# Performance work log

Hardware: AMD Instinct MI355X
Metric: run time of the kernel (lower is better)

## Reference

```python
import jax, jax.numpy as jnp
import numpy as np

B, LQ, LK = 8, 64, 256
E, H, D, NH = 128, 4, 32, 128  # embed_time, num_heads, input_dim, nhidden
EK = E // H


def setup_inputs() -> dict:
    key = jax.random.key(0)
    ks = jax.random.split(key, 10)
    s = 1.0 / np.sqrt(E)
    so = 1.0 / np.sqrt(D * H)
    return {
        "query": jax.random.normal(ks[0], (B, LQ, E), jnp.float32),
        "key": jax.random.normal(ks[1], (B, LK, E), jnp.float32),
        "value": jax.random.normal(ks[2], (B, LK, D), jnp.float32),
        "mask": jax.random.randint(ks[3], (B, LK, D), 0, 2, jnp.int32),
        "Wq": jax.random.uniform(ks[4], (E, E), jnp.float32, -s, s),
        "bq": jax.random.uniform(ks[5], (E,), jnp.float32, -s, s),
        "Wk": jax.random.uniform(ks[6], (E, E), jnp.float32, -s, s),
        "bk": jax.random.uniform(ks[7], (E,), jnp.float32, -s, s),
        "Wo": jax.random.uniform(ks[8], (D * H, NH), jnp.float32, -so, so),
        "bo": jax.random.uniform(ks[9], (NH,), jnp.float32, -so, so),
    }


def reference(query, key, value, mask, Wq, bq, Wk, bk, Wo, bo):
    # project and split heads: [B, L, E] -> [B, H, L, EK]
    q = (query @ Wq + bq).reshape(B, LQ, H, EK).transpose(0, 2, 1, 3)
    k = (key @ Wk + bk).reshape(B, LK, H, EK).transpose(0, 2, 1, 3)
    # scores: [B, H, LQ, LK]
    scores = jnp.einsum("bhqe,bhke->bhqk", q, k) / jnp.sqrt(jnp.asarray(EK, q.dtype))
    # per-feature masked logits: [B, H, LQ, LK, D] (broadcast, matches repeat_interleave)
    m = mask[:, None, None, :, :]  # [B,1,1,LK,D]
    logits = jnp.where(m == 0, jnp.asarray(-1e9, q.dtype), scores[..., None])
    p = jax.nn.softmax(logits, axis=-2)  # softmax over LK, per feature channel
    # weighted sum over LK: [B, H, LQ, D]
    x = jnp.sum(p * value[:, None, None, :, :], axis=-2)
    # merge heads: [B, LQ, H*D]
    x = x.transpose(0, 2, 1, 3).reshape(B, LQ, H * D)
    return x @ Wo + bo
```

## Files before the change

kernel.cpp:

```cpp
#include <hip/hip_runtime.h>

#define B_ 8
#define LQ_ 64
#define LK_ 256
#define E_ 128
#define H_ 4
#define D_ 32
#define NH_ 128
#define EK_ 32

__global__ __launch_bounds__(512) void fused_attn_kernel(
    const float* __restrict__ query, const float* __restrict__ key,
    const float* __restrict__ value, const int* __restrict__ mask,
    const float* __restrict__ Wq, const float* __restrict__ bq,
    const float* __restrict__ Wk,
    const float* __restrict__ Wo, const float* __restrict__ bo,
    float* __restrict__ out)
{
    const int blk = blockIdx.x;
    const int b  = blk >> 5;
    const int q0 = (blk & 31) * 2;
    const int t  = threadIdx.x;

    __shared__ float e_lds[8 * LK_];
    __shared__ float smem[9472];

    float* qrow  = smem;
    float* qpart = smem + 256;
    float* qp    = smem + 768;
    float* g     = smem + 1024;
    float* spart = smem + 2048;
    float* nump  = smem;
    float* denp  = smem + 4096;
    float* x     = smem + 8192;
    float* opart = smem + 8448;

    const int d  = t & 31;
    const int kg = t >> 5;
    float vv[16], mfv[16];
    {
        const float* vb = value + ((size_t)(b * LK_) + kg * 16) * D_ + d;
        const int*   mb = mask  + ((size_t)(b * LK_) + kg * 16) * D_ + d;
        #pragma unroll
        for (int j = 0; j < 16; ++j) {
            vv[j]  = vb[j * D_];
            mfv[j] = (float)mb[j * D_];
        }
    }

    if (t < 64) {
        reinterpret_cast<float4*>(qrow)[t] =
            reinterpret_cast<const float4*>(query + ((size_t)(b * LQ_) + q0) * E_)[t];
    }
    __syncthreads();

    {
        const int col = t & 127;
        const int z   = t >> 7;
        const int r   = z & 1;
        const int eh  = z >> 1;
        const float4* qr4 = reinterpret_cast<const float4*>(qrow + r * 128 + eh * 64);
        const float* wq = Wq + (size_t)(eh * 64) * E_ + col;
        float acc = 0.0f;
        #pragma unroll
        for (int j = 0; j < 16; ++j) {
            float4 qv = qr4[j];
            acc = fmaf(qv.x, wq[(size_t)(j * 4 + 0) * E_], acc);
            acc = fmaf(qv.y, wq[(size_t)(j * 4 + 1) * E_], acc);
            acc = fmaf(qv.z, wq[(size_t)(j * 4 + 2) * E_], acc);
            acc = fmaf(qv.w, wq[(size_t)(j * 4 + 3) * E_], acc);
        }
        qpart[z * 128 + col] = acc;
    }
    __syncthreads();

    if (t < 256) {
        const int col = t & 127, r = t >> 7;
        qp[r * 128 + col] =
            qpart[r * 128 + col] + qpart[(2 + r) * 128 + col] + bq[col];
    }
    __syncthreads();

    {
        const float inv_sqrt_ek = 0.17677669529663687f;
        const int e = t >> 2;
        const int p = t & 3;
        const float4* wk4 = reinterpret_cast<const float4*>(Wk + (size_t)e * E_ + p * EK_);
        float4 w[8];
        #pragma unroll
        for (int j = 0; j < 8; ++j) w[j] = wk4[j];
        #pragma unroll
        for (int r = 0; r < 2; ++r) {
            const float4* qp4 = reinterpret_cast<const float4*>(qp + r * 128 + p * EK_);
            float acc = 0.0f;
            #pragma unroll
            for (int j = 0; j < 8; ++j) {
                float4 pv = qp4[j];
                acc = fmaf(w[j].x, pv.x, acc);
                acc = fmaf(w[j].y, pv.y, acc);
                acc = fmaf(w[j].z, pv.z, acc);
                acc = fmaf(w[j].w, pv.w, acc);
            }
            g[(r * 4 + p) * 128 + e] = acc * inv_sqrt_ek;
        }
    }
    __syncthreads();

    {
        const int k  = t & 255;
        const int eh = t >> 8;
        const float4* kr =
            reinterpret_cast<const float4*>(key + ((size_t)(b * LK_) + k) * E_ + eh * 64);
        float acc[8] = {0.f, 0.f, 0.f, 0.f, 0.f, 0.f, 0.f, 0.f};
        #pragma unroll
        for (int j = 0; j < 16; ++j) {
            float4 kv = kr[j];
            #pragma unroll
            for (int rh = 0; rh < 8; ++rh) {
                float4 gg = reinterpret_cast<const float4*>(g + rh * 128 + eh * 64)[j];
                acc[rh] = fmaf(kv.x, gg.x, acc[rh]);
                acc[rh] = fmaf(kv.y, gg.y, acc[rh]);
                acc[rh] = fmaf(kv.z, gg.z, acc[rh]);
                acc[rh] = fmaf(kv.w, gg.w, acc[rh]);
            }
        }
        #pragma unroll
        for (int rh = 0; rh < 8; ++rh)
            spart[(eh * 8 + rh) * 256 + k] = acc[rh];
    }
    __syncthreads();

    {
        const int w = t >> 6;
        const int l = t & 63;
        float4 s0 = *reinterpret_cast<const float4*>(&spart[w * 256 + l * 4]);
        float4 s1 = *reinterpret_cast<const float4*>(&spart[(8 + w) * 256 + l * 4]);
        s0.x += s1.x; s0.y += s1.y; s0.z += s1.z; s0.w += s1.w;
        float m = fmaxf(fmaxf(s0.x, s0.y), fmaxf(s0.z, s0.w));
        #pragma unroll
        for (int off = 32; off; off >>= 1)
            m = fmaxf(m, __shfl_xor(m, off));
        float4 e;
        e.x = __expf(s0.x - m); e.y = __expf(s0.y - m);
        e.z = __expf(s0.z - m); e.w = __expf(s0.w - m);
        *reinterpret_cast<float4*>(&e_lds[w * LK_ + l * 4]) = e;
    }
    __syncthreads();

    {
        float num[8] = {0.f, 0.f, 0.f, 0.f, 0.f, 0.f, 0.f, 0.f};
        float den[8] = {0.f, 0.f, 0.f, 0.f, 0.f, 0.f, 0.f, 0.f};
        #pragma unroll
        for (int jq = 0; jq < 4; ++jq) {
            const float4 mv4 = make_float4(mfv[jq*4+0]*vv[jq*4+0], mfv[jq*4+1]*vv[jq*4+1],
                                           mfv[jq*4+2]*vv[jq*4+2], mfv[jq*4+3]*vv[jq*4+3]);
            const float4 mf4 = make_float4(mfv[jq*4+0], mfv[jq*4+1],
                                           mfv[jq*4+2], mfv[jq*4+3]);
            #pragma unroll
            for (int rh = 0; rh < 8; ++rh) {
                float4 ev = *reinterpret_cast<const float4*>(
                    &e_lds[rh * LK_ + kg * 16 + jq * 4]);
                num[rh] = fmaf(ev.x, mv4.x, num[rh]);
                num[rh] = fmaf(ev.y, mv4.y, num[rh]);
                num[rh] = fmaf(ev.z, mv4.z, num[rh]);
                num[rh] = fmaf(ev.w, mv4.w, num[rh]);
                den[rh] = fmaf(ev.x, mf4.x, den[rh]);
                den[rh] = fmaf(ev.y, mf4.y, den[rh]);
                den[rh] = fmaf(ev.z, mf4.z, den[rh]);
                den[rh] = fmaf(ev.w, mf4.w, den[rh]);
            }
        }
        #pragma unroll
        for (int rh = 0; rh < 8; ++rh) {
            nump[(kg * 8 + rh) * 32 + d] = num[rh];
            denp[(kg * 8 + rh) * 32 + d] = den[rh];
        }
    }
    __syncthreads();

    if (t < 256) {
        const int rh = t >> 5, dd = t & 31;
        float n = 0.f, dn = 0.f;
        #pragma unroll
        for (int k2 = 0; k2 < 16; ++k2) {
            n  += nump[(k2 * 8 + rh) * 32 + dd];
            dn += denp[(k2 * 8 + rh) * 32 + dd];
        }
        x[(rh >> 2) * 128 + (rh & 3) * 32 + dd] = n / dn;
    }
    __syncthreads();

    {
        const int col = t & 127;
        const int eq  = t >> 7;
        const int c0  = eq * 32;
        const float* wo = Wo + (size_t)c0 * NH_ + col;
        const float4* x40 = reinterpret_cast<const float4*>(x + c0);
        const float4* x41 = reinterpret_cast<const float4*>(x + 128 + c0);
        float acc0 = 0.f, acc1 = 0.f;
        #pragma unroll
        for (int j = 0; j < 8; ++j) {
            float4 xv0 = x40[j];
            float4 xv1 = x41[j];
            float w0 = wo[(size_t)(j * 4 + 0) * NH_];
            float w1 = wo[(size_t)(j * 4 + 1) * NH_];
            float w2 = wo[(size_t)(j * 4 + 2) * NH_];
            float w3 = wo[(size_t)(j * 4 + 3) * NH_];
            acc0 = fmaf(xv0.x, w0, acc0); acc1 = fmaf(xv1.x, w0, acc1);
            acc0 = fmaf(xv0.y, w1, acc0); acc1 = fmaf(xv1.y, w1, acc1);
            acc0 = fmaf(xv0.z, w2, acc0); acc1 = fmaf(xv1.z, w2, acc1);
            acc0 = fmaf(xv0.w, w3, acc0); acc1 = fmaf(xv1.w, w3, acc1);
        }
        opart[(eq * 2 + 0) * 128 + col] = acc0;
        opart[(eq * 2 + 1) * 128 + col] = acc1;
    }
    __syncthreads();

    if (t < 256) {
        const int col = t & 127, r = t >> 7;
        float s = bo[col];
        #pragma unroll
        for (int eq = 0; eq < 4; ++eq)
            s += opart[(eq * 2 + r) * 128 + col];
        out[((size_t)(b * LQ_) + q0 + r) * NH_ + col] = s;
    }
}

extern "C" void kernel_launch(void* const* d_in, const int* in_sizes, int n_in,
                              void* d_out, int out_size, void* d_ws, size_t ws_size,
                              hipStream_t stream) {
    const float* query = (const float*)d_in[0];
    const float* key   = (const float*)d_in[1];
    const float* value = (const float*)d_in[2];
    const int*   mask  = (const int*)d_in[3];
    const float* Wq    = (const float*)d_in[4];
    const float* bq    = (const float*)d_in[5];
    const float* Wk    = (const float*)d_in[6];
    const float* Wo    = (const float*)d_in[8];
    const float* bo    = (const float*)d_in[9];
    float* out = (float*)d_out;

    fused_attn_kernel<<<B_ * (LQ_ / 2), 512, 0, stream>>>(
        query, key, value, mask, Wq, bq, Wk, Wo, bo, out);
}
```

Baseline: 17.26 us.

## Stage key tile in swizzled LDS with coalesced prefetch and re-split score GEMM

Each block now loads the whole key tile for its batch with coalesced float4 loads at kernel start, holding it in registers while the Q projection runs. It then writes the tile into a large dynamic LDS buffer using an XOR swizzle. The score computation is re-split so each thread handles two key rows over a quarter of the embedding, reading keys from LDS instead of strided global rows, and the four partial sums are reduced afterwards. This requires about 136 KB of dynamic LDS and a one-time attribute call. It also adds register pressure from the staged float4s and an extra barrier, because the score partials alias the key buffer.

```diff
diff --git a/kernel.cpp b/kernel.cpp
--- a/kernel.cpp
+++ b/kernel.cpp
@@ -22,18 +22,26 @@
     const int q0 = (blk & 31) * 2;
     const int t  = threadIdx.x;
 
-    __shared__ float e_lds[8 * LK_];
-    __shared__ float smem[9472];
-
-    float* qrow  = smem;
-    float* qpart = smem + 256;
-    float* qp    = smem + 768;
-    float* g     = smem + 1024;
-    float* spart = smem + 2048;
-    float* nump  = smem;
-    float* denp  = smem + 4096;
-    float* x     = smem + 8192;
-    float* opart = smem + 8448;
+    extern __shared__ float dyn[];
+    float* qrow  = dyn;
+    float* qpart = dyn + 256;
+    float* qp    = dyn + 768;
+    float* g     = dyn + 1024;
+    float* kt    = dyn + 2048;
+    float* spart = dyn + 2048;
+    float* e_lds = dyn + 10240;
+    float* nump  = dyn + 12288;
+    float* denp  = dyn + 16384;
+    float* x     = dyn + 20480;
+    float* opart = dyn + 20736;
+
+    float4 st[16];
+    {
+        const float4* kb4 =
+            reinterpret_cast<const float4*>(key + (size_t)b * LK_ * E_);
+        #pragma unroll
+        for (int i = 0; i < 16; ++i) st[i] = kb4[i * 512 + t];
+    }
 
     const int d  = t & 31;
     const int kg = t >> 5;
@@ -71,6 +79,16 @@
             acc = fmaf(qv.w, wq[(size_t)(j * 4 + 3) * E_], acc);
         }
         qpart[z * 128 + col] = acc;
+    }
+    {
+        float4* kt4 = reinterpret_cast<float4*>(kt);
+        #pragma unroll
+        for (int i = 0; i < 16; ++i) {
+            const int n  = i * 512 + t;
+            const int kk = n >> 5;
+            const int jj = n & 31;
+            kt4[kk * 32 + (jj ^ (kk & 7))] = st[i];
+        }
     }
     __syncthreads();
 
@@ -106,36 +124,52 @@
     }
     __syncthreads();
 
-    {
-        const int k  = t & 255;
-        const int eh = t >> 8;
-        const float4* kr =
-            reinterpret_cast<const float4*>(key + ((size_t)(b * LK_) + k) * E_ + eh * 64);
-        float acc[8] = {0.f, 0.f, 0.f, 0.f, 0.f, 0.f, 0.f, 0.f};
-        #pragma unroll
-        for (int j = 0; j < 16; ++j) {
-            float4 kv = kr[j];
+    const int k5  = t & 127;
+    const int eq5 = t >> 7;
+    float acc0[8] = {0.f, 0.f, 0.f, 0.f, 0.f, 0.f, 0.f, 0.f};
+    float acc1[8] = {0.f, 0.f, 0.f, 0.f, 0.f, 0.f, 0.f, 0.f};
+    {
+        const int xr = k5 & 7;
+        const float4* kt4 = reinterpret_cast<const float4*>(kt);
+        const float4* g4  = reinterpret_cast<const float4*>(g);
+        #pragma unroll
+        for (int j = 0; j < 8; ++j) {
+            const int jj = eq5 * 8 + j;
+            const float4 kv0 = kt4[k5 * 32 + (jj ^ xr)];
+            const float4 kv1 = kt4[(k5 + 128) * 32 + (jj ^ xr)];
             #pragma unroll
             for (int rh = 0; rh < 8; ++rh) {
-                float4 gg = reinterpret_cast<const float4*>(g + rh * 128 + eh * 64)[j];
-                acc[rh] = fmaf(kv.x, gg.x, acc[rh]);
-                acc[rh] = fmaf(kv.y, gg.y, acc[rh]);
-                acc[rh] = fmaf(kv.z, gg.z, acc[rh]);
-                acc[rh] = fmaf(kv.w, gg.w, acc[rh]);
+                const float4 gg = g4[rh * 32 + jj];
+                acc0[rh] = fmaf(kv0.x, gg.x, acc0[rh]);
+                acc0[rh] = fmaf(kv0.y, gg.y, acc0[rh]);
+                acc0[rh] = fmaf(kv0.z, gg.z, acc0[rh]);
+                acc0[rh] = fmaf(kv0.w, gg.w, acc0[rh]);
+                acc1[rh] = fmaf(kv1.x, gg.x, acc1[rh]);
+                acc1[rh] = fmaf(kv1.y, gg.y, acc1[rh]);
+                acc1[rh] = fmaf(kv1.z, gg.z, acc1[rh]);
+                acc1[rh] = fmaf(kv1.w, gg.w, acc1[rh]);
             }
         }
-        #pragma unroll
-        for (int rh = 0; rh < 8; ++rh)
-            spart[(eh * 8 + rh) * 256 + k] = acc[rh];
+    }
+    __syncthreads();
+
+    #pragma unroll
+    for (int rh = 0; rh < 8; ++rh) {
+        spart[(eq5 * 8 + rh) * 256 + k5]       = acc0[rh];
+        spart[(eq5 * 8 + rh) * 256 + k5 + 128] = acc1[rh];
     }
     __syncthreads();
 
     {
         const int w = t >> 6;
         const int l = t & 63;
-        float4 s0 = *reinterpret_cast<const float4*>(&spart[w * 256 + l * 4]);
-        float4 s1 = *reinterpret_cast<const float4*>(&spart[(8 + w) * 256 + l * 4]);
-        s0.x += s1.x; s0.y += s1.y; s0.z += s1.z; s0.w += s1.w;
+        const float4* sp4 = reinterpret_cast<const float4*>(spart);
+        float4 s0 = sp4[w * 64 + l];
+        #pragma unroll
+        for (int eq = 1; eq < 4; ++eq) {
+            float4 s1 = sp4[(eq * 8 + w) * 64 + l];
+            s0.x += s1.x; s0.y += s1.y; s0.z += s1.z; s0.w += s1.w;
+        }
         float m = fmaxf(fmaxf(s0.x, s0.y), fmaxf(s0.z, s0.w));
         #pragma unroll
         for (int off = 32; off; off >>= 1)
@@ -197,7 +231,7 @@
         const float* wo = Wo + (size_t)c0 * NH_ + col;
         const float4* x40 = reinterpret_cast<const float4*>(x + c0);
         const float4* x41 = reinterpret_cast<const float4*>(x + 128 + c0);
-        float acc0 = 0.f, acc1 = 0.f;
+        float acc0o = 0.f, acc1o = 0.f;
         #pragma unroll
         for (int j = 0; j < 8; ++j) {
             float4 xv0 = x40[j];
@@ -206,13 +240,13 @@
             float w1 = wo[(size_t)(j * 4 + 1) * NH_];
             float w2 = wo[(size_t)(j * 4 + 2) * NH_];
             float w3 = wo[(size_t)(j * 4 + 3) * NH_];
-            acc0 = fmaf(xv0.x, w0, acc0); acc1 = fmaf(xv1.x, w0, acc1);
-            acc0 = fmaf(xv0.y, w1, acc0); acc1 = fmaf(xv1.y, w1, acc1);
-            acc0 = fmaf(xv0.z, w2, acc0); acc1 = fmaf(xv1.z, w2, acc1);
-            acc0 = fmaf(xv0.w, w3, acc0); acc1 = fmaf(xv1.w, w3, acc1);
-        }
-        opart[(eq * 2 + 0) * 128 + col] = acc0;
-        opart[(eq * 2 + 1) * 128 + col] = acc1;
+            acc0o = fmaf(xv0.x, w0, acc0o); acc1o = fmaf(xv1.x, w0, acc1o);
+            acc0o = fmaf(xv0.y, w1, acc0o); acc1o = fmaf(xv1.y, w1, acc1o);
+            acc0o = fmaf(xv0.z, w2, acc0o); acc1o = fmaf(xv1.z, w2, acc1o);
+            acc0o = fmaf(xv0.w, w3, acc0o); acc1o = fmaf(xv1.w, w3, acc1o);
+        }
+        opart[(eq * 2 + 0) * 128 + col] = acc0o;
+        opart[(eq * 2 + 1) * 128 + col] = acc1o;
     }
     __syncthreads();
 
@@ -240,6 +274,15 @@
     const float* bo    = (const float*)d_in[9];
     float* out = (float*)d_out;
 
-    fused_attn_kernel<<<B_ * (LQ_ / 2), 512, 0, stream>>>(
+    const size_t lds_bytes = 34816 * sizeof(float);
+    static bool attr_set = false;
+    if (!attr_set) {
+        hipFuncSetAttribute(reinterpret_cast<const void*>(fused_attn_kernel),
+                            hipFuncAttributeMaxDynamicSharedMemorySize,
+                            (int)lds_bytes);
+        attr_set = true;
+    }
+
+    fused_attn_kernel<<<B_ * (LQ_ / 2), 512, lds_bytes, stream>>>(
         query, key, value, mask, Wq, bq, Wk, Wo, bo, out);
 }
```

New measurement: 27.76 us. +60.8%, slower.
